# Kernel optimization log

Hardware: AMD Instinct MI355X
Metric: run time of the kernel (lower is better)

## Reference

```python
import jax, jax.numpy as jnp
import numpy as np

H = 64
IN_DIM = 32
N = 50000
E = 100000
B = 500


def setup_inputs() -> dict:
    key = jax.random.key(0)
    ks = jax.random.split(key, 16)
    def rn(k, shape, s=0.05):
        return jax.random.normal(k, shape, dtype=jnp.float32) * s
    inp = dict(
        nfeat=rn(ks[0], (N, IN_DIM), 1.0),
        efeat=rn(ks[1], (E, 5), 1.0),
        lin0_w=rn(ks[2], (IN_DIM, H)), lin0_b=jnp.zeros((H,), jnp.float32),
        ew1=rn(ks[3], (5, 128)), eb1=jnp.zeros((128,), jnp.float32),
        ew2=rn(ks[4], (128, H * H)), eb2=jnp.zeros((H * H,), jnp.float32),
        conv_b=jnp.zeros((H,), jnp.float32),
        gru_wih=rn(ks[5], (3 * H, H)), gru_whh=rn(ks[6], (3 * H, H)),
        gru_bih=jnp.zeros((3 * H,), jnp.float32), gru_bhh=jnp.zeros((3 * H,), jnp.float32),
        lstm_wih=rn(ks[7], (4 * H, 2 * H)), lstm_whh=rn(ks[8], (4 * H, H)),
        lstm_bih=jnp.zeros((4 * H,), jnp.float32), lstm_bhh=jnp.zeros((4 * H,), jnp.float32),
        fc1_w=rn(ks[9], (2 * H, H)), fc1_b=jnp.zeros((H,), jnp.float32),
        fc2_w=rn(ks[10], (H, 1)), fc2_b=jnp.zeros((1,), jnp.float32),
        src=jax.random.randint(ks[11], (E,), 0, N),
        dst=jax.random.randint(ks[12], (E,), 0, N),
        graph_id=jnp.arange(N) // (N // B),  # B graphs of equal size, sorted
        num_graphs=B,
    )
    return inp


def reference(nfeat, efeat, lin0_w, lin0_b, ew1, eb1, ew2, eb2, conv_b,
              gru_wih, gru_whh, gru_bih, gru_bhh,
              lstm_wih, lstm_whh, lstm_bih, lstm_bhh,
              fc1_w, fc1_b, fc2_w, fc2_b,
              src, dst, graph_id, num_graphs):
    n_nodes = nfeat.shape[0]
    # lin0 + relu
    h = jax.nn.relu(nfeat @ lin0_w + lin0_b)  # [N, H]
    # edge-conditioned weight matrices (same for all 3 iterations)
    We = (jax.nn.relu(efeat @ ew1 + eb1) @ ew2 + eb2).reshape(-1, H, H)  # [E, H, H]
    deg = jnp.maximum(
        jax.ops.segment_sum(jnp.ones(src.shape[0], jnp.float32), dst, num_segments=n_nodes), 1.0)
    for _ in range(3):
        # NNConv: gather src feats, per-edge matmul, scatter-mean at dst
        msg = jnp.einsum('eh,eho->eo', h[src], We)  # [E, H]
        agg = jax.ops.segment_sum(msg, dst, num_segments=n_nodes) / deg[:, None]
        m = jax.nn.relu(agg + conv_b)
        # GRU step (PyTorch gate order r,z,n)
        gi = m @ gru_wih.T + gru_bih
        gh = h @ gru_whh.T + gru_bhh
        r = jax.nn.sigmoid(gi[:, :H] + gh[:, :H])
        z = jax.nn.sigmoid(gi[:, H:2 * H] + gh[:, H:2 * H])
        n = jnp.tanh(gi[:, 2 * H:] + r * gh[:, 2 * H:])
        h = (1.0 - z) * n + z * h
    feat = h  # [N, H]
    # Set2Set pooling: 3 iters, 1-layer LSTM with input 2H
    q_star = jnp.zeros((num_graphs, 2 * H), jnp.float32)
    hh = jnp.zeros((num_graphs, H), jnp.float32)
    cc = jnp.zeros((num_graphs, H), jnp.float32)
    for _ in range(3):
        gates = q_star @ lstm_wih.T + lstm_bih + hh @ lstm_whh.T + lstm_bhh
        i = jax.nn.sigmoid(gates[:, :H])
        f = jax.nn.sigmoid(gates[:, H:2 * H])
        g = jnp.tanh(gates[:, 2 * H:3 * H])
        o = jax.nn.sigmoid(gates[:, 3 * H:])
        cc = f * cc + i * g
        hh = o * jnp.tanh(cc)
        q = hh  # [B, H]
        e = jnp.sum(feat * q[graph_id], axis=-1)  # [N]
        emax = jax.ops.segment_max(e, graph_id, num_segments=num_graphs)
        alpha = jnp.exp(e - emax[graph_id])
        denom = jax.ops.segment_sum(alpha, graph_id, num_segments=num_graphs)
        alpha = alpha / denom[graph_id]
        readout = jax.ops.segment_sum(alpha[:, None] * feat, graph_id, num_segments=num_graphs)
        q_star = jnp.concatenate([q, readout], axis=-1)  # [B, 2H]
    pred = jax.nn.relu(q_star @ fc1_w + fc1_b) @ fc2_w + fc2_b  # [B, 1]
    return pred.reshape(-1)
```

## Files before the change

kernel.cpp:

```cpp
#include <hip/hip_runtime.h>

#define HD 64
#define NNODE 50000
#define NEDGE 100000
#define NGR 500
#define NPG 100
#define EPAD 100352
#define NCH 66

typedef _Float16 f16;
typedef _Float16 f16x2 __attribute__((ext_vector_type(2)));
typedef _Float16 f16x8 __attribute__((ext_vector_type(8)));
typedef float f32x4 __attribute__((ext_vector_type(4)));
typedef float f32x16 __attribute__((ext_vector_type(16)));

__device__ __forceinline__ float sigmoidf_(float x) { return 1.f / (1.f + __expf(-x)); }

#define G_NODE 12500
#define G_EMLP 3136
#define G_PACK 2112
#define G_GRU  48
#define G_T1   128
#define G_T2   64
#define G_IDX  392
#define G_ALL (G_NODE + G_EMLP + G_PACK + G_GRU + G_T1 + G_T2 + G_IDX)

__global__ __launch_bounds__(256) void k_prep_all(
    const float* __restrict__ nfeat, const float* __restrict__ lin0_w, const float* __restrict__ lin0_b,
    const float* __restrict__ efeat, const float* __restrict__ ew1, const float* __restrict__ eb1,
    const float* __restrict__ ew2, const float* __restrict__ eb2,
    const float* __restrict__ gwih, const float* __restrict__ gwhh,
    const float* __restrict__ lwih, const float* __restrict__ lwhh,
    const int* __restrict__ src, const int* __restrict__ dst,
    float* __restrict__ h, f16* __restrict__ uE, f16* __restrict__ w2hp,
    f16* __restrict__ gB1, f16* __restrict__ gB2,
    float* __restrict__ lwihT, float* __restrict__ lwhhT,
    int* __restrict__ srcP, int* __restrict__ dstP, int* __restrict__ cnt) {
    int bb = blockIdx.x;
    int t = threadIdx.x;
    if (bb < G_NODE) {
        int idx = bb * 256 + t;
        int n = idx >> 6, o = idx & 63;
        if (n >= NNODE) return;
        const float* nf = nfeat + n * 32;
        float acc = lin0_b[o];
#pragma unroll
        for (int i = 0; i < 32; i++) acc += nf[i] * lin0_w[i * 64 + o];
        h[idx] = fmaxf(acc, 0.f);
        return;
    }
    bb -= G_NODE;
    if (bb < G_EMLP) {
        __shared__ float sw[5 * 128];
        __shared__ float sb[128];
        for (int idx = t; idx < 640; idx += 256) sw[idx] = ew1[idx];
        if (t < 128) sb[t] = eb1[t];
        __syncthreads();
        int idx = bb * 256 + t;
        int e = idx >> 3, grp = idx & 7;
        bool valid = e < NEDGE;
        float ef[5];
#pragma unroll
        for (int i = 0; i < 5; i++) ef[i] = valid ? efeat[e * 5 + i] : 0.f;
        f16x8 v0, v1;
#pragma unroll
        for (int s = 0; s < 8; s++) {
            int k = grp * 16 + s;
            float acc = sb[k];
#pragma unroll
            for (int i = 0; i < 5; i++) acc += ef[i] * sw[i * 128 + k];
            v0[s] = valid ? (f16)fmaxf(acc, 0.f) : (f16)0.f;
        }
#pragma unroll
        for (int s = 0; s < 8; s++) {
            int k = grp * 16 + 8 + s;
            float acc = sb[k];
#pragma unroll
            for (int i = 0; i < 5; i++) acc += ef[i] * sw[i * 128 + k];
            v1[s] = valid ? (f16)fmaxf(acc, 0.f) : (f16)0.f;
        }
        *(f16x8*)(uE + (size_t)e * 128 + grp * 16) = v0;
        *(f16x8*)(uE + (size_t)e * 128 + grp * 16 + 8) = v1;
        return;
    }
    bb -= G_EMLP;
    if (bb < G_PACK) {
        int idx = bb * 256 + t;
        int q = idx & 7;
        int F = idx >> 3;
        int l = F & 63;
        int ks = (F >> 6) & 7;
        int ch = (F >> 9) & 1;
        int c = F >> 10;
        int kg = c * 128 + ks * 16 + (l >> 5) * 8 + q;
        int n = ch * 32 + (l & 31);
        float v = 0.f;
        if (kg < 8192) v = ew2[kg * 64 + n];
        else if (kg < 8256) v = eb2[(kg - 8192) * 64 + n];
        w2hp[idx] = (f16)v;
        return;
    }
    bb -= G_PACK;
    if (bb < G_GRU) {
        int idx = bb * 256 + t;
        int cp = idx >> 6, k = idx & 63;
        int w = cp / 48, rem = cp % 48;
        int tg = rem >> 4, cc = rem & 15;
        int orow = tg * 64 + w * 16 + cc;
        gB1[idx] = (f16)gwih[orow * 64 + k];
        gB2[idx] = (f16)gwhh[orow * 64 + k];
        return;
    }
    bb -= G_GRU;
    if (bb < G_T1) {
        int idx = bb * 256 + t;
        int r = idx >> 7, c = idx & 127;
        lwihT[c * 256 + r] = lwih[idx];
        return;
    }
    bb -= G_T1;
    if (bb < G_T2) {
        int idx = bb * 256 + t;
        int r = idx >> 6, c = idx & 63;
        lwhhT[c * 256 + r] = lwhh[idx];
        return;
    }
    bb -= G_T2;
    {
        int e = bb * 256 + t;
        if (e >= EPAD) return;
        if (e < NEDGE) {
            int d = dst[e];
            srcP[e] = src[e];
            dstP[e] = d;
            atomicAdd(&cnt[d], 1);
        } else {
            srcP[e] = 0;
            dstP[e] = -1;
        }
    }
}

__global__ void k_deg_inv(const int* __restrict__ cnt, float* __restrict__ dinv) {
    int n = blockIdx.x * 256 + threadIdx.x;
    if (n < NNODE) dinv[n] = 1.f / (float)max(cnt[n], 1);
}

#define MSG_STEP(BCUR, BNXT, CC)                                                                   \
    {                                                                                              \
        const f16x8* bp = gBp + (size_t)(g4 + (CC) + 1) * 1024;                                    \
        _Pragma("unroll") for (int ks = 0; ks < 8; ks++) BNXT[ks] = bp[ks * 64];                   \
        _Pragma("unroll") for (int ks = 0; ks < 8; ks++) {                                         \
            _Pragma("unroll") for (int i = 0; i < 4; i++) {                                        \
                f16 uu = uc[i][((CC) << 1) | (ks >> 2)];                                           \
                f16x8 av = xf[i][ks & 3] * uu;                                                     \
                acc[i] = __builtin_amdgcn_mfma_f32_32x32x16_f16(av, BCUR[ks], acc[i], 0, 0, 0);    \
            }                                                                                      \
        }                                                                                          \
    }

__global__ __launch_bounds__(64, 2) void k_msg_fused(
    const float* __restrict__ h, const f16* __restrict__ uE, const f16* __restrict__ w2hp,
    const int* __restrict__ srcP, const int* __restrict__ dstP, float* __restrict__ agg) {
    int l = threadIdx.x;
    int wid = blockIdx.x;
    int eb = (wid >> 1) * 128;
    int ch = wid & 1;
    int lm = l & 31, hi = l >> 5;
    f16x8 xf[4][4];
#pragma unroll
    for (int i = 0; i < 4; i++) {
        const float* xb = h + (size_t)srcP[eb + i * 32 + lm] * 64;
#pragma unroll
        for (int h4 = 0; h4 < 4; h4++) {
            float4 v0 = *(const float4*)(xb + h4 * 16 + hi * 8);
            float4 v1 = *(const float4*)(xb + h4 * 16 + hi * 8 + 4);
            f16x8 xv;
            xv[0] = (f16)v0.x; xv[1] = (f16)v0.y; xv[2] = (f16)v0.z; xv[3] = (f16)v0.w;
            xv[4] = (f16)v1.x; xv[5] = (f16)v1.y; xv[6] = (f16)v1.z; xv[7] = (f16)v1.w;
            xf[i][h4] = xv;
        }
    }
    const f16x8* gBp = (const f16x8*)w2hp + ch * 512 + l;
    const f16x8* up[4];
#pragma unroll
    for (int i = 0; i < 4; i++) up[i] = (const f16x8*)(uE + (size_t)(eb + i * 32 + lm) * 128);
    f32x16 acc[4];
#pragma unroll
    for (int i = 0; i < 4; i++)
#pragma unroll
        for (int r = 0; r < 16; r++) acc[i][r] = 0.f;
    f16x8 bA[8], bB[8];
#pragma unroll
    for (int ks = 0; ks < 8; ks++) bA[ks] = gBp[ks * 64];
    f16x8 uc[4], un[4];
#pragma unroll
    for (int i = 0; i < 4; i++) uc[i] = up[i][0];
#pragma unroll 1
    for (int g = 0; g < 16; g++) {
        int g4 = g * 4;
        int gn = (g < 15) ? g + 1 : 15;
#pragma unroll
        for (int i = 0; i < 4; i++) un[i] = up[i][gn];
        MSG_STEP(bA, bB, 0)
        MSG_STEP(bB, bA, 1)
        MSG_STEP(bA, bB, 2)
        MSG_STEP(bB, bA, 3)
#pragma unroll
        for (int i = 0; i < 4; i++) uc[i] = un[i];
    }
#pragma unroll
    for (int ks = 0; ks < 4; ks++)
#pragma unroll
        for (int i = 0; i < 4; i++)
            acc[i] = __builtin_amdgcn_mfma_f32_32x32x16_f16(xf[i][ks], bA[ks], acc[i], 0, 0, 0);
#pragma unroll
    for (int i = 0; i < 4; i++) {
        int rbase = eb + i * 32 + 4 * hi;
#pragma unroll
        for (int b = 0; b < 4; b++) {
            int4 d4 = *(const int4*)(dstP + rbase + 8 * b);
#pragma unroll
            for (int rr = 0; rr < 4; rr++) {
                int d = (rr == 0) ? d4.x : (rr == 1) ? d4.y : (rr == 2) ? d4.z : d4.w;
                float v = acc[i][b * 4 + rr];
                if (d >= 0) atomicAdd(agg + (size_t)d * 64 + ch * 32 + lm, v);
            }
        }
    }
}

#define GWP 72
__global__ __launch_bounds__(256) void k_gru2(float* __restrict__ agg,
                                              const float* __restrict__ dinv,
                                              const float* __restrict__ convb,
                                              const f16* __restrict__ B1g,
                                              const f16* __restrict__ B2g,
                                              const float* __restrict__ bih,
                                              const float* __restrict__ bhh,
                                              float* __restrict__ h) {
    __shared__ f16 sM[64 * GWP];
    __shared__ f16 sH[64 * GWP];
    int t = threadIdx.x;
    int nb = blockIdx.x * 64;
    int w = t >> 6, l = t & 63, lr = l & 15, lg = l >> 4;
    f16x8 b1[2][3], b2[2][3];
#pragma unroll
    for (int kk = 0; kk < 2; kk++)
#pragma unroll
        for (int j = 0; j < 3; j++) {
            size_t off = (size_t)(w * 48 + j * 16 + lr) * 64 + kk * 32 + lg * 8;
            b1[kk][j] = *(const f16x8*)(B1g + off);
            b2[kk][j] = *(const f16x8*)(B2g + off);
        }
#pragma unroll
    for (int it = 0; it < 16; it++) {
        int idx = t + 256 * it;
        int node = idx >> 6, k = idx & 63;
        int gn = nb + node;
        float mv = 0.f, hv = 0.f;
        if (gn < NNODE) {
            size_t off = (size_t)gn * 64 + k;
            mv = fmaxf(agg[off] * dinv[gn] + convb[k], 0.f);
            hv = h[off];
            agg[off] = 0.f;
        }
        sM[node * GWP + k] = (f16)mv;
        sH[node * GWP + k] = (f16)hv;
    }
    __syncthreads();
    f32x4 aih[4][3], ahh[4][3];
#pragma unroll
    for (int i = 0; i < 4; i++)
#pragma unroll
        for (int j = 0; j < 3; j++) {
            aih[i][j] = (f32x4){0.f, 0.f, 0.f, 0.f};
            ahh[i][j] = (f32x4){0.f, 0.f, 0.f, 0.f};
        }
#pragma unroll
    for (int kk = 0; kk < 2; kk++) {
        f16x8 am[4], ah[4];
#pragma unroll
        for (int i = 0; i < 4; i++) {
            am[i] = *(const f16x8*)(sM + (i * 16 + lr) * GWP + kk * 32 + lg * 8);
            ah[i] = *(const f16x8*)(sH + (i * 16 + lr) * GWP + kk * 32 + lg * 8);
        }
#pragma unroll
        for (int i = 0; i < 4; i++)
#pragma unroll
            for (int j = 0; j < 3; j++) {
                aih[i][j] = __builtin_amdgcn_mfma_f32_16x16x32_f16(am[i], b1[kk][j], aih[i][j], 0, 0, 0);
                ahh[i][j] = __builtin_amdgcn_mfma_f32_16x16x32_f16(ah[i], b2[kk][j], ahh[i][j], 0, 0, 0);
            }
    }
    float bi0 = bih[0 * 64 + w * 16 + lr], bh0 = bhh[0 * 64 + w * 16 + lr];
    float bi1 = bih[1 * 64 + w * 16 + lr], bh1 = bhh[1 * 64 + w * 16 + lr];
    float bi2 = bih[2 * 64 + w * 16 + lr], bh2 = bhh[2 * 64 + w * 16 + lr];
#pragma unroll
    for (int i = 0; i < 4; i++)
#pragma unroll
        for (int r = 0; r < 4; r++) {
            int node = i * 16 + lg * 4 + r;
            int gn = nb + node;
            if (gn >= NNODE) continue;
            float rg = sigmoidf_(aih[i][0][r] + bi0 + ahh[i][0][r] + bh0);
            float z = sigmoidf_(aih[i][1][r] + bi1 + ahh[i][1][r] + bh1);
            float nn = tanhf(aih[i][2][r] + bi2 + rg * (ahh[i][2][r] + bh2));
            size_t off = (size_t)gn * 64 + w * 16 + lr;
            float hold = h[off];
            h[off] = (1.f - z) * nn + z * hold;
        }
}

#define FP 68
__global__ __launch_bounds__(256) void k_s2s(const float* __restrict__ feat,
                                             const float* __restrict__ wihT,
                                             const float* __restrict__ whhT,
                                             const float* __restrict__ lbih,
                                             const float* __restrict__ lbhh,
                                             const float* __restrict__ fc1w,
                                             const float* __restrict__ fc1b,
                                             const float* __restrict__ fc2w,
                                             const float* __restrict__ fc2b,
                                             float* __restrict__ out) {
    __shared__ float sf[NPG * FP];
    __shared__ float sq[128];
    __shared__ float sh[64], scc[64];
    __shared__ float sg[256];
    __shared__ float se[NPG];
    __shared__ float red[2];
    int g = blockIdx.x, t = threadIdx.x;
    const float* fb = feat + (size_t)g * NPG * 64;
    for (int idx = t; idx < NPG * 64; idx += 256)
        sf[(idx >> 6) * FP + (idx & 63)] = fb[idx];
    if (t < 128) sq[t] = 0.f;
    if (t >= 128 && t < 192) { sh[t - 128] = 0.f; scc[t - 128] = 0.f; }
    __syncthreads();
    for (int it = 0; it < 3; it++) {
        float gate = lbih[t] + lbhh[t];
#pragma unroll 8
        for (int i = 0; i < 128; i++) gate += sq[i] * wihT[i * 256 + t];
#pragma unroll 8
        for (int i = 0; i < 64; i++) gate += sh[i] * whhT[i * 256 + t];
        sg[t] = gate;
        __syncthreads();
        if (t < 64) {
            float ig = sigmoidf_(sg[t]);
            float fg = sigmoidf_(sg[64 + t]);
            float gg = tanhf(sg[128 + t]);
            float og = sigmoidf_(sg[192 + t]);
            float c = fg * scc[t] + ig * gg;
            scc[t] = c;
            float hv = og * tanhf(c);
            sh[t] = hv;
            sq[t] = hv;
        }
        __syncthreads();
        if (t < NPG) {
            float e = 0.f;
#pragma unroll 8
            for (int o = 0; o < 64; o++) e += sf[t * FP + o] * sh[o];
            se[t] = e;
        }
        __syncthreads();
        if (t < 64) {
            float m = -1e30f;
            for (int i2 = t; i2 < NPG; i2 += 64) m = fmaxf(m, se[i2]);
            for (int d = 32; d; d >>= 1) m = fmaxf(m, __shfl_down(m, d));
            if (t == 0) red[0] = m;
        }
        __syncthreads();
        float emax = red[0];
        if (t < NPG) se[t] = __expf(se[t] - emax);
        __syncthreads();
        if (t < 64) {
            float s = 0.f;
            for (int i2 = t; i2 < NPG; i2 += 64) s += se[i2];
            for (int d = 32; d; d >>= 1) s += __shfl_down(s, d);
            if (t == 0) red[1] = s;
        }
        __syncthreads();
        if (t < 64) {
            float dnv = 1.f / red[1];
            float r = 0.f;
#pragma unroll 4
            for (int n = 0; n < NPG; n++) r += se[n] * sf[n * FP + t];
            sq[64 + t] = r * dnv;
        }
        __syncthreads();
    }
    if (t < 64) {
        float hsum = fc1b[t];
#pragma unroll 8
        for (int i = 0; i < 128; i++) hsum += sq[i] * fc1w[i * 64 + t];
        float p = fmaxf(hsum, 0.f) * fc2w[t];
        for (int d = 32; d; d >>= 1) p += __shfl_down(p, d);
        if (t == 0) out[g] = p + fc2b[0];
    }
}

extern "C" void kernel_launch(void* const* d_in, const int* in_sizes, int n_in,
                              void* d_out, int out_size, void* d_ws, size_t ws_size,
                              hipStream_t stream) {
    const float* nfeat = (const float*)d_in[0];
    const float* efeat = (const float*)d_in[1];
    const float* lin0_w = (const float*)d_in[2];
    const float* lin0_b = (const float*)d_in[3];
    const float* ew1 = (const float*)d_in[4];
    const float* eb1 = (const float*)d_in[5];
    const float* ew2 = (const float*)d_in[6];
    const float* eb2 = (const float*)d_in[7];
    const float* convb = (const float*)d_in[8];
    const float* gwih = (const float*)d_in[9];
    const float* gwhh = (const float*)d_in[10];
    const float* gbih = (const float*)d_in[11];
    const float* gbhh = (const float*)d_in[12];
    const float* lwih = (const float*)d_in[13];
    const float* lwhh = (const float*)d_in[14];
    const float* lbih = (const float*)d_in[15];
    const float* lbhh = (const float*)d_in[16];
    const float* fc1w = (const float*)d_in[17];
    const float* fc1b = (const float*)d_in[18];
    const float* fc2w = (const float*)d_in[19];
    const float* fc2b = (const float*)d_in[20];
    const int* src = (const int*)d_in[21];
    const int* dst = (const int*)d_in[22];
    float* out = (float*)d_out;

    char* p = (char*)d_ws;
    auto alloc = [&](size_t bytes) {
        char* q = p;
        p += (bytes + 255) & ~(size_t)255;
        return q;
    };
    f16* uE = (f16*)alloc((size_t)EPAD * 128 * 2 + 256);
    f16* w2hp = (f16*)alloc((size_t)540672 * 2);
    float* h = (float*)alloc((size_t)NNODE * 64 * 4);
    float* agg = (float*)alloc((size_t)NNODE * 64 * 4);
    int* cnt = (int*)alloc((size_t)NNODE * 4);
    float* dinv = (float*)alloc((size_t)NNODE * 4);
    float* lwihT = (float*)alloc((size_t)128 * 256 * 4);
    float* lwhhT = (float*)alloc((size_t)64 * 256 * 4);
    f16* gB1 = (f16*)alloc((size_t)12288 * 2);
    f16* gB2 = (f16*)alloc((size_t)12288 * 2);
    int* srcP = (int*)alloc((size_t)EPAD * 4);
    int* dstP = (int*)alloc((size_t)EPAD * 4);
    if ((size_t)(p - (char*)d_ws) > ws_size) return;

    hipMemsetAsync(cnt, 0, (size_t)NNODE * 4, stream);
    hipMemsetAsync(agg, 0, (size_t)NNODE * 64 * 4, stream);

    k_prep_all<<<G_ALL, 256, 0, stream>>>(nfeat, lin0_w, lin0_b, efeat, ew1, eb1, ew2, eb2,
                                          gwih, gwhh, lwih, lwhh, src, dst,
                                          h, uE, w2hp, gB1, gB2, lwihT, lwhhT, srcP, dstP, cnt);
    k_deg_inv<<<(NNODE + 255) / 256, 256, 0, stream>>>(cnt, dinv);

    for (int it = 0; it < 3; it++) {
        k_msg_fused<<<(EPAD / 128) * 2, 64, 0, stream>>>(h, uE, w2hp, srcP, dstP, agg);
        k_gru2<<<(NNODE + 63) / 64, 256, 0, stream>>>(agg, dinv, convb, gB1, gB2, gbih, gbhh, h);
    }
    k_s2s<<<NGR, 256, 0, stream>>>(h, lwihT, lwhhT, lbih, lbhh, fc1w, fc1b, fc2w, fc2b, out);
}
```

Before: 545.9 us.

## Switch message kernel to 16x16x32 MFMA with 3-deep B prefetch and new packing

The fused NNConv message kernel moves from 32x32x16 MFMA tiles to 16x16x32 tiles. Each wave now holds 8 row tiles of 16 edges with two 16-column output halves, and B chunks are prefetched three deep through four rotating register buffers. The weight repacking moves out of the prep kernel into a dedicated kernel that stages through shared memory so global reads are coalesced, using a layout matched to the new MFMA shape. Occupancy drops to one wave per SIMD via launch bounds, and register pressure rises.

```diff
diff --git a/kernel.cpp b/kernel.cpp
--- a/kernel.cpp
+++ b/kernel.cpp
@@ -12,27 +12,24 @@
 typedef _Float16 f16x2 __attribute__((ext_vector_type(2)));
 typedef _Float16 f16x8 __attribute__((ext_vector_type(8)));
 typedef float f32x4 __attribute__((ext_vector_type(4)));
-typedef float f32x16 __attribute__((ext_vector_type(16)));
 
 __device__ __forceinline__ float sigmoidf_(float x) { return 1.f / (1.f + __expf(-x)); }
 
 #define G_NODE 12500
 #define G_EMLP 3136
-#define G_PACK 2112
 #define G_GRU  48
 #define G_T1   128
 #define G_T2   64
 #define G_IDX  392
-#define G_ALL (G_NODE + G_EMLP + G_PACK + G_GRU + G_T1 + G_T2 + G_IDX)
+#define G_ALL (G_NODE + G_EMLP + G_GRU + G_T1 + G_T2 + G_IDX)
 
 __global__ __launch_bounds__(256) void k_prep_all(
     const float* __restrict__ nfeat, const float* __restrict__ lin0_w, const float* __restrict__ lin0_b,
     const float* __restrict__ efeat, const float* __restrict__ ew1, const float* __restrict__ eb1,
-    const float* __restrict__ ew2, const float* __restrict__ eb2,
     const float* __restrict__ gwih, const float* __restrict__ gwhh,
     const float* __restrict__ lwih, const float* __restrict__ lwhh,
     const int* __restrict__ src, const int* __restrict__ dst,
-    float* __restrict__ h, f16* __restrict__ uE, f16* __restrict__ w2hp,
+    float* __restrict__ h, f16* __restrict__ uE,
     f16* __restrict__ gB1, f16* __restrict__ gB2,
     float* __restrict__ lwihT, float* __restrict__ lwhhT,
     int* __restrict__ srcP, int* __restrict__ dstP, int* __restrict__ cnt) {
@@ -84,23 +81,6 @@
         return;
     }
     bb -= G_EMLP;
-    if (bb < G_PACK) {
-        int idx = bb * 256 + t;
-        int q = idx & 7;
-        int F = idx >> 3;
-        int l = F & 63;
-        int ks = (F >> 6) & 7;
-        int ch = (F >> 9) & 1;
-        int c = F >> 10;
-        int kg = c * 128 + ks * 16 + (l >> 5) * 8 + q;
-        int n = ch * 32 + (l & 31);
-        float v = 0.f;
-        if (kg < 8192) v = ew2[kg * 64 + n];
-        else if (kg < 8256) v = eb2[(kg - 8192) * 64 + n];
-        w2hp[idx] = (f16)v;
-        return;
-    }
-    bb -= G_PACK;
     if (bb < G_GRU) {
         int idx = bb * 256 + t;
         int cp = idx >> 6, k = idx & 63;
@@ -141,90 +121,129 @@
     }
 }
 
+__global__ __launch_bounds__(256) void k_pack_b(const float* __restrict__ ew2,
+                                                const float* __restrict__ eb2,
+                                                f16* __restrict__ w2hp) {
+    __shared__ float s[8192];
+    int c = blockIdx.x, t = threadIdx.x;
+    for (int i = t; i < 8192; i += 256) {
+        int kg = c * 128 + (i >> 6);
+        float v = 0.f;
+        if (kg < 8192) v = ew2[(size_t)c * 8192 + i];
+        else if (kg < 8256) v = eb2[(kg - 8192) * 64 + (i & 63)];
+        s[i] = v;
+    }
+    __syncthreads();
+    f16* outp = w2hp + (size_t)c * 8192 + t * 32;
+#pragma unroll
+    for (int ff = 0; ff < 4; ff++) {
+        int F = t * 4 + ff;
+        int l = F & 63, ks = (F >> 6) & 3, ch2 = F >> 8;
+        int sl = (F >> 8) & 3;
+        int jj = (F >> 6) & 3;
+        (void)ks; (void)ch2;
+        f16x8 v;
+#pragma unroll
+        for (int q = 0; q < 8; q++)
+            v[q] = (f16)s[(sl * 32 + ((l >> 4) << 3) + q) * 64 + jj * 16 + (l & 15)];
+        *(f16x8*)(outp + ff * 8) = v;
+    }
+}
+
 __global__ void k_deg_inv(const int* __restrict__ cnt, float* __restrict__ dinv) {
     int n = blockIdx.x * 256 + threadIdx.x;
     if (n < NNODE) dinv[n] = 1.f / (float)max(cnt[n], 1);
 }
 
-#define MSG_STEP(BCUR, BNXT, CC)                                                                   \
-    {                                                                                              \
-        const f16x8* bp = gBp + (size_t)(g4 + (CC) + 1) * 1024;                                    \
-        _Pragma("unroll") for (int ks = 0; ks < 8; ks++) BNXT[ks] = bp[ks * 64];                   \
-        _Pragma("unroll") for (int ks = 0; ks < 8; ks++) {                                         \
-            _Pragma("unroll") for (int i = 0; i < 4; i++) {                                        \
-                f16 uu = uc[i][((CC) << 1) | (ks >> 2)];                                           \
-                f16x8 av = xf[i][ks & 3] * uu;                                                     \
-                acc[i] = __builtin_amdgcn_mfma_f32_32x32x16_f16(av, BCUR[ks], acc[i], 0, 0, 0);    \
-            }                                                                                      \
-        }                                                                                          \
-    }
-
-__global__ __launch_bounds__(64, 2) void k_msg_fused(
+#define ISSUE(BUF, CN)                                                                  \
+    {                                                                                   \
+        const f16x8* bp = gBp + (size_t)(CN) * 1024;                                    \
+        _Pragma("unroll") for (int s = 0; s < 8; s++)                                   \
+            BUF[s] = bp[(s >> 1) * 256 + (s & 1) * 64];                                 \
+    }
+#define COMP(BUF, CL)                                                                   \
+    {                                                                                   \
+        _Pragma("unroll") for (int sl = 0; sl < 4; sl++)                                \
+            _Pragma("unroll") for (int i = 0; i < 8; i++) {                             \
+                f16x8 av = xf[i][sl & 1] * uc[i][2 * (CL) + (sl >> 1)];                 \
+                acc[i][0] = __builtin_amdgcn_mfma_f32_16x16x32_f16(av, BUF[sl * 2], acc[i][0], 0, 0, 0);     \
+                acc[i][1] = __builtin_amdgcn_mfma_f32_16x16x32_f16(av, BUF[sl * 2 + 1], acc[i][1], 0, 0, 0); \
+            }                                                                           \
+    }
+
+__global__ __launch_bounds__(64, 1) void k_msg_fused(
     const float* __restrict__ h, const f16* __restrict__ uE, const f16* __restrict__ w2hp,
     const int* __restrict__ srcP, const int* __restrict__ dstP, float* __restrict__ agg) {
     int l = threadIdx.x;
     int wid = blockIdx.x;
     int eb = (wid >> 1) * 128;
     int ch = wid & 1;
-    int lm = l & 31, hi = l >> 5;
-    f16x8 xf[4][4];
-#pragma unroll
-    for (int i = 0; i < 4; i++) {
-        const float* xb = h + (size_t)srcP[eb + i * 32 + lm] * 64;
-#pragma unroll
-        for (int h4 = 0; h4 < 4; h4++) {
-            float4 v0 = *(const float4*)(xb + h4 * 16 + hi * 8);
-            float4 v1 = *(const float4*)(xb + h4 * 16 + hi * 8 + 4);
+    int lr = l & 15, lg = l >> 4;
+    f16x8 xf[8][2];
+#pragma unroll
+    for (int i = 0; i < 8; i++) {
+        const float* xb = h + (size_t)srcP[eb + i * 16 + lr] * 64;
+#pragma unroll
+        for (int p = 0; p < 2; p++) {
+            float4 v0 = *(const float4*)(xb + p * 32 + lg * 8);
+            float4 v1 = *(const float4*)(xb + p * 32 + lg * 8 + 4);
             f16x8 xv;
             xv[0] = (f16)v0.x; xv[1] = (f16)v0.y; xv[2] = (f16)v0.z; xv[3] = (f16)v0.w;
             xv[4] = (f16)v1.x; xv[5] = (f16)v1.y; xv[6] = (f16)v1.z; xv[7] = (f16)v1.w;
-            xf[i][h4] = xv;
-        }
-    }
-    const f16x8* gBp = (const f16x8*)w2hp + ch * 512 + l;
-    const f16x8* up[4];
-#pragma unroll
-    for (int i = 0; i < 4; i++) up[i] = (const f16x8*)(uE + (size_t)(eb + i * 32 + lm) * 128);
-    f32x16 acc[4];
-#pragma unroll
-    for (int i = 0; i < 4; i++)
-#pragma unroll
-        for (int r = 0; r < 16; r++) acc[i][r] = 0.f;
-    f16x8 bA[8], bB[8];
-#pragma unroll
-    for (int ks = 0; ks < 8; ks++) bA[ks] = gBp[ks * 64];
-    f16x8 uc[4], un[4];
-#pragma unroll
-    for (int i = 0; i < 4; i++) uc[i] = up[i][0];
+            xf[i][p] = xv;
+        }
+    }
+    const f16x8* gBp = (const f16x8*)w2hp + ch * 128 + l;
+    f32x4 acc[8][2];
+#pragma unroll
+    for (int i = 0; i < 8; i++) {
+        acc[i][0] = (f32x4){0.f, 0.f, 0.f, 0.f};
+        acc[i][1] = (f32x4){0.f, 0.f, 0.f, 0.f};
+    }
+    f16x8 b0[8], b1[8], b2[8], b3[8], bz[4];
+    ISSUE(b0, 0)
+    ISSUE(b1, 1)
+    ISSUE(b2, 2)
+#pragma unroll
+    for (int s = 0; s < 4; s++)
+        bz[s] = gBp[(size_t)64 * 1024 + (s >> 1) * 256 + (s & 1) * 64];
+    f16x8 uc[8], un[8];
+#pragma unroll
+    for (int i = 0; i < 8; i++)
+        uc[i] = *((const f16x8*)(uE + (size_t)(eb + i * 16 + lr) * 128));
 #pragma unroll 1
-    for (int g = 0; g < 16; g++) {
-        int g4 = g * 4;
-        int gn = (g < 15) ? g + 1 : 15;
-#pragma unroll
-        for (int i = 0; i < 4; i++) un[i] = up[i][gn];
-        MSG_STEP(bA, bB, 0)
-        MSG_STEP(bB, bA, 1)
-        MSG_STEP(bA, bB, 2)
-        MSG_STEP(bB, bA, 3)
-#pragma unroll
-        for (int i = 0; i < 4; i++) uc[i] = un[i];
-    }
-#pragma unroll
-    for (int ks = 0; ks < 4; ks++)
-#pragma unroll
-        for (int i = 0; i < 4; i++)
-            acc[i] = __builtin_amdgcn_mfma_f32_32x32x16_f16(xf[i][ks], bA[ks], acc[i], 0, 0, 0);
-#pragma unroll
-    for (int i = 0; i < 4; i++) {
-        int rbase = eb + i * 32 + 4 * hi;
-#pragma unroll
-        for (int b = 0; b < 4; b++) {
-            int4 d4 = *(const int4*)(dstP + rbase + 8 * b);
-#pragma unroll
-            for (int rr = 0; rr < 4; rr++) {
-                int d = (rr == 0) ? d4.x : (rr == 1) ? d4.y : (rr == 2) ? d4.z : d4.w;
-                float v = acc[i][b * 4 + rr];
-                if (d >= 0) atomicAdd(agg + (size_t)d * 64 + ch * 32 + lm, v);
+    for (int it = 0; it < 15; it++) {
+        int c = it * 4;
+#pragma unroll
+        for (int i = 0; i < 8; i++)
+            un[i] = *((const f16x8*)(uE + (size_t)(eb + i * 16 + lr) * 128) + (it + 1));
+        ISSUE(b3, c + 3) COMP(b0, 0)
+        ISSUE(b0, c + 4) COMP(b1, 1)
+        ISSUE(b1, c + 5) COMP(b2, 2)
+        ISSUE(b2, c + 6) COMP(b3, 3)
+#pragma unroll
+        for (int i = 0; i < 8; i++) uc[i] = un[i];
+    }
+    ISSUE(b3, 63)
+    COMP(b0, 0) COMP(b1, 1) COMP(b2, 2) COMP(b3, 3)
+#pragma unroll
+    for (int sl = 0; sl < 2; sl++)
+#pragma unroll
+        for (int i = 0; i < 8; i++) {
+            acc[i][0] = __builtin_amdgcn_mfma_f32_16x16x32_f16(xf[i][sl], bz[sl * 2], acc[i][0], 0, 0, 0);
+            acc[i][1] = __builtin_amdgcn_mfma_f32_16x16x32_f16(xf[i][sl], bz[sl * 2 + 1], acc[i][1], 0, 0, 0);
+        }
+#pragma unroll
+    for (int i = 0; i < 8; i++) {
+        int rb = eb + i * 16 + lg * 4;
+        int4 d4 = *(const int4*)(dstP + rb);
+#pragma unroll
+        for (int r = 0; r < 4; r++) {
+            int d = (r == 0) ? d4.x : (r == 1) ? d4.y : (r == 2) ? d4.z : d4.w;
+            if (d >= 0) {
+                float* ap = agg + (size_t)d * 64 + ch * 32 + lr;
+                atomicAdd(ap, acc[i][0][r]);
+                atomicAdd(ap + 16, acc[i][1][r]);
             }
         }
     }
@@ -434,7 +453,7 @@
         return q;
     };
     f16* uE = (f16*)alloc((size_t)EPAD * 128 * 2 + 256);
-    f16* w2hp = (f16*)alloc((size_t)540672 * 2);
+    f16* w2hp = (f16*)alloc((size_t)NCH * 8192 * 2);
     float* h = (float*)alloc((size_t)NNODE * 64 * 4);
     float* agg = (float*)alloc((size_t)NNODE * 64 * 4);
     int* cnt = (int*)alloc((size_t)NNODE * 4);
@@ -450,9 +469,10 @@
     hipMemsetAsync(cnt, 0, (size_t)NNODE * 4, stream);
     hipMemsetAsync(agg, 0, (size_t)NNODE * 64 * 4, stream);
 
-    k_prep_all<<<G_ALL, 256, 0, stream>>>(nfeat, lin0_w, lin0_b, efeat, ew1, eb1, ew2, eb2,
+    k_prep_all<<<G_ALL, 256, 0, stream>>>(nfeat, lin0_w, lin0_b, efeat, ew1, eb1,
                                           gwih, gwhh, lwih, lwhh, src, dst,
-                                          h, uE, w2hp, gB1, gB2, lwihT, lwhhT, srcP, dstP, cnt);
+                                          h, uE, gB1, gB2, lwihT, lwhhT, srcP, dstP, cnt);
+    k_pack_b<<<NCH, 256, 0, stream>>>(ew2, eb2, w2hp);
     k_deg_inv<<<(NNODE + 255) / 256, 256, 0, stream>>>(cnt, dinv);
 
     for (int it = 0; it < 3; it++) {
```

New measurement: 566.0 us. +3.7%, slower.
